# Kernel optimization log

Hardware: AMD Instinct MI355X
Metric: run time of the kernel (lower is better)

## Reference

```python
import jax, jax.numpy as jnp
import numpy as np

B, S, D, H = 4, 2048, 1024, 16
HD = D // H  # head_dim = 64


def setup_inputs() -> dict:
    key = jax.random.key(0)
    ks = jax.random.split(key, 5)
    scale = 0.02
    x = jax.random.normal(ks[0], (B, S, D), dtype=jnp.float32)
    W_qkv = jax.random.normal(ks[1], (D, 3 * D), dtype=jnp.float32) * scale
    b_qkv = jnp.zeros((3 * D,), dtype=jnp.float32)
    W_out = jax.random.normal(ks[2], (D, D), dtype=jnp.float32) * scale
    b_out = jnp.zeros((D,), dtype=jnp.float32)
    return {"x": x, "W_qkv": W_qkv, "b_qkv": b_qkv, "W_out": W_out, "b_out": b_out}


def reference(x, W_qkv, b_qkv, W_out, b_out):
    b, s, d = x.shape
    qkv = x @ W_qkv + b_qkv                      # [B,S,3D]
    q, k, v = jnp.split(qkv, 3, axis=-1)
    # [B,S,D] -> [B,H,S,hd]
    q = q.reshape(b, s, H, HD).transpose(0, 2, 1, 3)
    k = k.reshape(b, s, H, HD).transpose(0, 2, 1, 3)
    v = v.reshape(b, s, H, HD).transpose(0, 2, 1, 3)
    scores = jnp.einsum('bhqd,bhkd->bhqk', q, k) / jnp.sqrt(jnp.float32(HD))
    causal = jnp.tril(jnp.ones((s, s), dtype=bool))  # [S,S]
    scores = jnp.where(causal[None, None], scores, -jnp.inf)
    probs = jax.nn.softmax(scores, axis=-1)
    # dropout is identity in eval mode
    attn = jnp.einsum('bhqk,bhkd->bhqd', probs, v)  # [B,H,S,hd]
    attn = attn.transpose(0, 2, 1, 3).reshape(b, s, d)
    return attn @ W_out + b_out
```

## Files before the change

kernel.cpp:

```cpp
#include <hip/hip_runtime.h>


typedef short s16;
typedef __attribute__((ext_vector_type(4))) short s16x4;
typedef __attribute__((ext_vector_type(8))) short bf16x8;
typedef __attribute__((ext_vector_type(4))) float f32x4;

__device__ __forceinline__ s16 f2bf(float f) {
    union { float f; unsigned int i; } v;
    v.f = f;
    unsigned int r = v.i + 0x7fffu + ((v.i >> 16) & 1u);
    return (s16)(r >> 16);
}

__device__ __forceinline__ unsigned pack_bf16(float a, float b) {
    union { float f; unsigned u; } x, y;
    x.f = a; y.f = b;
    return __byte_perm(x.u + 0x8000u, y.u + 0x8000u, 0x7632);
}

__device__ __forceinline__ void load_lds16(const s16* g, s16* lds_base) {
    __builtin_amdgcn_global_load_lds(
        (const __attribute__((address_space(1))) void*)g,
        (__attribute__((address_space(3))) void*)lds_base, 16, 0, 0);
}

template <int N>
__device__ __forceinline__ void waitcnt_vm() {
    if constexpr (N == 0)      asm volatile("s_waitcnt vmcnt(0)" ::: "memory");
    else if constexpr (N == 3) asm volatile("s_waitcnt vmcnt(3)" ::: "memory");
    else if constexpr (N == 5) asm volatile("s_waitcnt vmcnt(5)" ::: "memory");
}

__global__ __launch_bounds__(256) void prep(
    const float* __restrict__ x,    s16* __restrict__ xo,
    const float* __restrict__ Wq,   s16* __restrict__ oq,
    const float* __restrict__ Wo,   s16* __restrict__ oo) {
    const int bid = blockIdx.x;
    const int tid = threadIdx.x;
    if (bid < 8192) {
        const int i = (bid * 256 + tid) * 4;
        const float4 f = *(const float4*)(x + i);
        s16x4 r = {f2bf(f.x), f2bf(f.y), f2bf(f.z), f2bf(f.w)};
        *(s16x4*)(xo + i) = r;
        return;
    }
    __shared__ float tile[32][33];
    const float* in;
    s16* out;
    int C, bx, by;
    if (bid < 11264) {
        const int b = bid - 8192;
        in = Wq; out = oq; C = 3072; bx = b % 96; by = b / 96;
    } else {
        const int b = bid - 11264;
        in = Wo; out = oo; C = 1024; bx = b & 31; by = b >> 5;
    }
    const int R = 1024;
    const int cb = bx * 32, rb = by * 32;
    const int tx = tid & 31, ty = tid >> 5;
#pragma unroll
    for (int i = 0; i < 32; i += 8)
        tile[ty + i][tx] = in[(size_t)(rb + ty + i) * C + cb + tx];
    __syncthreads();
#pragma unroll
    for (int i = 0; i < 32; i += 8)
        out[(size_t)(cb + ty + i) * R + rb + tx] = f2bf(tile[tx][ty + i]);
}

template <bool OUT_F32, int ACH, int BCH, int NWN_L2, int MF, int NF>
__global__ __launch_bounds__(512, 2) void gemm_tb(
    const s16* __restrict__ A,
    const s16* __restrict__ Bt,
    const float* __restrict__ bias,
    void* __restrict__ Cv,
    int M, int N, int K, int gx) {
    constexpr int NWN   = 1 << NWN_L2;
    constexpr int LOADS = ACH + BCH;
    constexpr int ABUF  = ACH * 4096;
    constexpr int BBUF  = BCH * 4096;
    constexpr int BM = ACH * 128, BN = BCH * 128;
    static_assert(MF * 16 * (8 / NWN) == BM, "M geometry");
    static_assert(NF * 16 * NWN == BN, "N geometry");
    __shared__ __attribute__((aligned(16))) s16 As[3 * ABUF];
    __shared__ __attribute__((aligned(16))) s16 Bs[3 * BBUF];

    const int tid  = threadIdx.x;
    const int lane = tid & 63;
    const int wave = tid >> 6;
    const int l15  = lane & 15;
    const int quad = lane >> 4;
    const int wr   = wave >> NWN_L2;
    const int wc   = wave & (NWN - 1);

    const int cpx = (int)gridDim.x >> 3;
    const int bid = (int)blockIdx.x;
    const int swz = (bid & 7) * cpx + (bid >> 3);
    const int m0 = (swz / gx) * BM;
    const int n0 = (swz % gx) * BN;

    const int sr  = tid >> 2;
    const int gl  = tid & 3;
    const int gsw = gl ^ ((sr >> 1) & 3);
    const s16* Ag = A  + (size_t)(m0 + sr) * K + gsw * 8;
    const s16* Bg = Bt + (size_t)(n0 + sr) * K + gsw * 8;

#define STG(bufi, kt) do {                                                          \
    _Pragma("unroll")                                                               \
    for (int c = 0; c < ACH; ++c)                                                   \
        load_lds16(Ag + (size_t)c * 128 * K + (size_t)(kt) * 32,                    \
                   &As[(bufi) * ABUF + c * 4096 + wave * 512]);                     \
    _Pragma("unroll")                                                               \
    for (int c = 0; c < BCH; ++c)                                                   \
        load_lds16(Bg + (size_t)c * 128 * K + (size_t)(kt) * 32,                    \
                   &Bs[(bufi) * BBUF + c * 4096 + wave * 512]); } while (0)

    f32x4 acc[MF][NF];
#pragma unroll
    for (int i = 0; i < MF; ++i)
#pragma unroll
        for (int j = 0; j < NF; ++j)
            acc[i][j] = (f32x4){0.f, 0.f, 0.f, 0.f};

    const int nk = K >> 5;

    STG(0, 0);
    STG(1, 1);
    waitcnt_vm<LOADS>();
    __builtin_amdgcn_s_barrier();

    for (int t = 0; t < nk; ++t) {
        const int cur = t % 3;
        if (t + 2 < nk) STG((t + 2) % 3, t + 2);

        const s16* Ab = As + cur * ABUF;
        const s16* Bb = Bs + cur * BBUF;
        bf16x8 bf[NF];
#pragma unroll
        for (int nf = 0; nf < NF; ++nf) {
            const int row = wc * (NF * 16) + nf * 16 + l15;
            bf[nf] = *(const bf16x8*)(Bb + row * 32 + ((quad ^ ((row >> 1) & 3)) << 3));
        }
        __builtin_amdgcn_s_setprio(1);
#pragma unroll
        for (int mf = 0; mf < MF; ++mf) {
            const int row = wr * (MF * 16) + mf * 16 + l15;
            const bf16x8 af = *(const bf16x8*)(Ab + row * 32 + ((quad ^ ((row >> 1) & 3)) << 3));
#pragma unroll
            for (int nf = 0; nf < NF; ++nf)
                acc[mf][nf] = __builtin_amdgcn_mfma_f32_16x16x32_bf16(af, bf[nf], acc[mf][nf], 0, 0, 0);
        }
        __builtin_amdgcn_s_setprio(0);

        if (t + 2 < nk)      waitcnt_vm<LOADS>();
        else if (t + 1 < nk) waitcnt_vm<0>();
        if (t + 1 < nk) __builtin_amdgcn_s_barrier();
    }
#undef STG

    float bv[NF];
#pragma unroll
    for (int nf = 0; nf < NF; ++nf)
        bv[nf] = bias[n0 + wc * (NF * 16) + nf * 16 + l15];
#pragma unroll
    for (int mf = 0; mf < MF; ++mf) {
#pragma unroll
        for (int r = 0; r < 4; ++r) {
            const int row = m0 + wr * (MF * 16) + mf * 16 + quad * 4 + r;
#pragma unroll
            for (int nf = 0; nf < NF; ++nf) {
                const int col = n0 + wc * (NF * 16) + nf * 16 + l15;
                const float v = acc[mf][nf][r] + bv[nf];
                if constexpr (OUT_F32)
                    ((float*)Cv)[(size_t)row * N + col] = v;
                else
                    ((s16*)Cv)[(size_t)row * N + col] = f2bf(v);
            }
        }
    }
}

__global__ __launch_bounds__(256) void attn_fwd(
    const s16* __restrict__ qkv,
    s16* __restrict__ attn) {
    __shared__ __attribute__((aligned(16))) s16 Ks[64 * 72];
    __shared__ __attribute__((aligned(16))) s16 Vt[64 * 72];
    __shared__ __attribute__((aligned(16))) s16 PT[4][32][88];

    const int tid  = threadIdx.x;
    const int lane = tid & 63;
    const int wave = tid >> 6;
    const int l15  = lane & 15;
    const int quad = lane >> 4;

    const int bid = blockIdx.x;
    const int hi  = bid >> 8;
    const int a   = bid & 3;
    const int bh  = (bid >> 2) & 63;
    const int qbase = a * 2 + (hi >> 1);
    const int qt  = (hi & 1) ? 15 - qbase : qbase;

    const size_t rowbase = (size_t)(bh >> 4) * 2048;
    const int hoff = (bh & 15) * 64;
    const int kp  = tid >> 3;
    const int p_s = tid & 7;
    const int kg  = kp >> 2;

    const float C2 = 0.18033688011112042f;
    const float M2 = 12.0f;

    const int wq = qt * 128 + wave * 32;

    bf16x8 qf[2][2];
#pragma unroll
    for (int qs = 0; qs < 2; ++qs)
#pragma unroll
        for (int ks = 0; ks < 2; ++ks)
            qf[qs][ks] = *(const bf16x8*)(qkv + (rowbase + wq + qs * 16 + l15) * 3072 + hoff + ks * 32 + quad * 8);

    float l_lane[2] = {0.f, 0.f};
    f32x4 o[2][4];
#pragma unroll
    for (int qs = 0; qs < 2; ++qs)
#pragma unroll
        for (int hs = 0; hs < 4; ++hs)
            o[qs][hs] = (f32x4){0.f, 0.f, 0.f, 0.f};

    const int nkt = qt * 2 + 2;
    bf16x8 kv[2], vv[2];
#pragma unroll
    for (int dk = 0; dk < 2; ++dk) {
        const s16* g = qkv + (rowbase + 2 * kp + dk) * 3072 + hoff + p_s * 8;
        kv[dk] = *(const bf16x8*)(g + 1024);
        vv[dk] = *(const bf16x8*)(g + 2048);
    }

    for (int kt = 0; kt < nkt; ++kt) {
        const int k0 = kt * 64;
        __syncthreads();
#pragma unroll
        for (int dk = 0; dk < 2; ++dk)
            *(bf16x8*)(Ks + (2 * kp + dk) * 72 + p_s * 8) = kv[dk];
#pragma unroll
        for (int j = 0; j < 8; ++j) {
            const unsigned dw = (unsigned)(unsigned short)vv[0][j] |
                                ((unsigned)(unsigned short)vv[1][j] << 16);
            *(unsigned*)(Vt + (p_s * 8 + j) * 72 + ((kg ^ p_s) << 3) + (2 * kp & 7)) = dw;
        }
        __syncthreads();

        if (kt + 1 < nkt) {
#pragma unroll
            for (int dk = 0; dk < 2; ++dk) {
                const s16* g = qkv + (rowbase + k0 + 64 + 2 * kp + dk) * 3072 + hoff + p_s * 8;
                kv[dk] = *(const bf16x8*)(g + 1024);
                vv[dk] = *(const bf16x8*)(g + 2048);
            }
        }

        if (k0 > wq + 31) continue;

        f32x4 st[2][4];
#pragma unroll
        for (int qs = 0; qs < 2; ++qs)
#pragma unroll
            for (int kb = 0; kb < 4; ++kb)
                st[qs][kb] = (f32x4){0.f, 0.f, 0.f, 0.f};
        __builtin_amdgcn_s_setprio(1);
#pragma unroll
        for (int kb = 0; kb < 4; ++kb)
#pragma unroll
            for (int ks = 0; ks < 2; ++ks) {
                const bf16x8 kf = *(const bf16x8*)(Ks + (kb * 16 + l15) * 72 + ks * 32 + quad * 8);
#pragma unroll
                for (int qs = 0; qs < 2; ++qs)
                    st[qs][kb] = __builtin_amdgcn_mfma_f32_16x16x32_bf16(kf, qf[qs][ks], st[qs][kb], 0, 0, 0);
            }
        __builtin_amdgcn_s_setprio(0);

        const bool edge = (k0 + 63 > wq);
#pragma unroll
        for (int qs = 0; qs < 2; ++qs) {
            const int q = wq + qs * 16 + l15;
#pragma unroll
            for (int kb = 0; kb < 4; ++kb) {
                float p4[4];
#pragma unroll
                for (int r = 0; r < 4; ++r) {
                    float t = fmaf(st[qs][kb][r], C2, -M2);
                    if (edge) {
                        const int key = k0 + kb * 16 + quad * 4 + r;
                        t = (key <= q) ? t : -150.f;
                    }
                    p4[r] = __builtin_amdgcn_exp2f(t);
                    l_lane[qs] += p4[r];
                }
                uint2 dd;
                dd.x = pack_bf16(p4[0], p4[1]);
                dd.y = pack_bf16(p4[2], p4[3]);
                *(uint2*)(&PT[wave][qs * 16 + l15][kb * 16 + quad * 4]) = dd;
            }
        }

        __builtin_amdgcn_s_setprio(1);
#pragma unroll
        for (int kk = 0; kk < 2; ++kk) {
            bf16x8 pf[2];
#pragma unroll
            for (int qs = 0; qs < 2; ++qs)
                pf[qs] = *(const bf16x8*)(&PT[wave][qs * 16 + l15][kk * 32 + quad * 8]);
#pragma unroll
            for (int hs = 0; hs < 4; ++hs) {
                const bf16x8 vf = *(const bf16x8*)(
                    Vt + (hs * 16 + l15) * 72 + (((kk * 4 + quad) ^ (2 * hs + (l15 >> 3))) << 3));
#pragma unroll
                for (int qs = 0; qs < 2; ++qs)
                    o[qs][hs] = __builtin_amdgcn_mfma_f32_16x16x32_bf16(vf, pf[qs], o[qs][hs], 0, 0, 0);
            }
        }
        __builtin_amdgcn_s_setprio(0);
    }

    float rl[2];
#pragma unroll
    for (int qs = 0; qs < 2; ++qs) {
        float l = l_lane[qs];
        l += __shfl_xor(l, 16);
        l += __shfl_xor(l, 32);
        rl[qs] = 1.f / l;
    }

#pragma unroll
    for (int qs = 0; qs < 2; ++qs) {
        const int q = wq + qs * 16 + l15;
#pragma unroll
        for (int hs = 0; hs < 4; ++hs) {
            uint2 dd;
            dd.x = pack_bf16(o[qs][hs][0] * rl[qs], o[qs][hs][1] * rl[qs]);
            dd.y = pack_bf16(o[qs][hs][2] * rl[qs], o[qs][hs][3] * rl[qs]);
            *(uint2*)(attn + (rowbase + q) * 1024 + hoff + hs * 16 + quad * 4) = dd;
        }
    }
}

extern "C" void kernel_launch(void* const* d_in, const int* in_sizes, int n_in,
                              void* d_out, int out_size, void* d_ws, size_t ws_size,
                              hipStream_t stream) {
    const float* x    = (const float*)d_in[0];
    const float* Wqkv = (const float*)d_in[1];
    const float* bqkv = (const float*)d_in[2];
    const float* Wout = (const float*)d_in[3];
    const float* bout = (const float*)d_in[4];
    float* out = (float*)d_out;

    s16* ws   = (s16*)d_ws;
    s16* qkv  = ws;
    s16* xba  = qkv + (size_t)8192 * 3072;
    s16* wtq  = xba + (size_t)8192 * 1024;
    s16* wto  = wtq + (size_t)3072 * 1024;

    prep<<<12288, 256, 0, stream>>>(x, xba, Wqkv, wtq, Wout, wto);
    gemm_tb<false, 2, 3, 2, 8, 6><<<256, 512, 0, stream>>>(
        xba, wtq, bqkv, qkv, 8192, 3072, 1024, 8);
    attn_fwd<<<1024, 256, 0, stream>>>(qkv, xba);
    gemm_tb<true, 2, 1, 1, 4, 4><<<256, 512, 0, stream>>>(
        xba, wto, bout, out, 8192, 1024, 1024, 8);
}
```

Baseline: 258.6 us.

## Replace GEMM with 4-slot ring-buffered, split-phase pipelined kernel

```diff
diff --git a/kernel.cpp b/kernel.cpp
--- a/kernel.cpp
+++ b/kernel.cpp
@@ -29,7 +29,7 @@
 __device__ __forceinline__ void waitcnt_vm() {
     if constexpr (N == 0)      asm volatile("s_waitcnt vmcnt(0)" ::: "memory");
     else if constexpr (N == 3) asm volatile("s_waitcnt vmcnt(3)" ::: "memory");
-    else if constexpr (N == 5) asm volatile("s_waitcnt vmcnt(5)" ::: "memory");
+    else if constexpr (N == 4) asm volatile("s_waitcnt vmcnt(4)" ::: "memory");
 }
 
 __global__ __launch_bounds__(256) void prep(
@@ -68,35 +68,33 @@
         out[(size_t)(cb + ty + i) * R + rb + tx] = f2bf(tile[tx][ty + i]);
 }
 
-template <bool OUT_F32, int ACH, int BCH, int NWN_L2, int MF, int NF>
-__global__ __launch_bounds__(512, 2) void gemm_tb(
+template <bool OUT_F32, int BCH>
+__global__ __launch_bounds__(512, 2) void gemm_ring(
     const s16* __restrict__ A,
     const s16* __restrict__ Bt,
     const float* __restrict__ bias,
     void* __restrict__ Cv,
     int M, int N, int K, int gx) {
-    constexpr int NWN   = 1 << NWN_L2;
-    constexpr int LOADS = ACH + BCH;
-    constexpr int ABUF  = ACH * 4096;
-    constexpr int BBUF  = BCH * 4096;
-    constexpr int BM = ACH * 128, BN = BCH * 128;
-    static_assert(MF * 16 * (8 / NWN) == BM, "M geometry");
-    static_assert(NF * 16 * NWN == BN, "N geometry");
-    __shared__ __attribute__((aligned(16))) s16 As[3 * ABUF];
-    __shared__ __attribute__((aligned(16))) s16 Bs[3 * BBUF];
+    constexpr int BN    = BCH * 128;
+    constexpr int NF    = BCH * 2;
+    constexpr int LPK   = 2 + BCH;
+    constexpr int ASLOT = 256 * 32;
+    constexpr int BSLOT = BN * 32;
+    __shared__ __attribute__((aligned(16))) s16 As[4 * ASLOT];
+    __shared__ __attribute__((aligned(16))) s16 Bs[4 * BSLOT];
 
     const int tid  = threadIdx.x;
     const int lane = tid & 63;
     const int wave = tid >> 6;
     const int l15  = lane & 15;
     const int quad = lane >> 4;
-    const int wr   = wave >> NWN_L2;
-    const int wc   = wave & (NWN - 1);
+    const int wr   = wave >> 2;
+    const int wc   = wave & 3;
 
     const int cpx = (int)gridDim.x >> 3;
     const int bid = (int)blockIdx.x;
     const int swz = (bid & 7) * cpx + (bid >> 3);
-    const int m0 = (swz / gx) * BM;
+    const int m0 = (swz / gx) * 256;
     const int n0 = (swz % gx) * BN;
 
     const int sr  = tid >> 2;
@@ -105,68 +103,87 @@
     const s16* Ag = A  + (size_t)(m0 + sr) * K + gsw * 8;
     const s16* Bg = Bt + (size_t)(n0 + sr) * K + gsw * 8;
 
-#define STG(bufi, kt) do {                                                          \
-    _Pragma("unroll")                                                               \
-    for (int c = 0; c < ACH; ++c)                                                   \
-        load_lds16(Ag + (size_t)c * 128 * K + (size_t)(kt) * 32,                    \
-                   &As[(bufi) * ABUF + c * 4096 + wave * 512]);                     \
-    _Pragma("unroll")                                                               \
-    for (int c = 0; c < BCH; ++c)                                                   \
-        load_lds16(Bg + (size_t)c * 128 * K + (size_t)(kt) * 32,                    \
-                   &Bs[(bufi) * BBUF + c * 4096 + wave * 512]); } while (0)
-
-    f32x4 acc[MF][NF];
-#pragma unroll
-    for (int i = 0; i < MF; ++i)
+    auto stgA = [&](int slot, int kt) {
+        load_lds16(Ag + (size_t)kt * 32,           &As[slot * ASLOT + wave * 512]);
+        load_lds16(Ag + (size_t)128 * K + kt * 32, &As[slot * ASLOT + 4096 + wave * 512]);
+    };
+    auto stgB = [&](int slot, int kt) {
+        load_lds16(Bg + (size_t)kt * 32, &Bs[slot * BSLOT + wave * 512]);
+        if constexpr (BCH == 2)
+            load_lds16(Bg + (size_t)128 * K + kt * 32, &Bs[slot * BSLOT + 4096 + wave * 512]);
+    };
+
+    f32x4 acc[8][NF];
+#pragma unroll
+    for (int i = 0; i < 8; ++i)
 #pragma unroll
         for (int j = 0; j < NF; ++j)
             acc[i][j] = (f32x4){0.f, 0.f, 0.f, 0.f};
 
     const int nk = K >> 5;
-
-    STG(0, 0);
-    STG(1, 1);
-    waitcnt_vm<LOADS>();
+    const int gr = ((quad ^ ((l15 >> 1) & 3)) << 3);
+
+    stgA(0, 0); stgB(0, 0);
+    stgA(1, 1); stgB(1, 1);
+    waitcnt_vm<LPK>();
     __builtin_amdgcn_s_barrier();
 
-    for (int t = 0; t < nk; ++t) {
-        const int cur = t % 3;
-        if (t + 2 < nk) STG((t + 2) % 3, t + 2);
-
-        const s16* Ab = As + cur * ABUF;
-        const s16* Bb = Bs + cur * BBUF;
-        bf16x8 bf[NF];
-#pragma unroll
-        for (int nf = 0; nf < NF; ++nf) {
-            const int row = wc * (NF * 16) + nf * 16 + l15;
-            bf[nf] = *(const bf16x8*)(Bb + row * 32 + ((quad ^ ((row >> 1) & 3)) << 3));
-        }
-        __builtin_amdgcn_s_setprio(1);
-#pragma unroll
-        for (int mf = 0; mf < MF; ++mf) {
-            const int row = wr * (MF * 16) + mf * 16 + l15;
-            const bf16x8 af = *(const bf16x8*)(Ab + row * 32 + ((quad ^ ((row >> 1) & 3)) << 3));
+    for (int tq = 0; tq < nk; tq += 4) {
+#pragma unroll
+        for (int u = 0; u < 4; ++u) {
+            const int t = tq + u;
+            const s16* Ab = As + u * ASLOT;
+            const s16* Bb = Bs + u * BSLOT;
+            const bool pre = (t + 2 < nk);
+            const int ns = (t + 2) & 3;
+
+            bf16x8 bf[NF], af[4];
 #pragma unroll
             for (int nf = 0; nf < NF; ++nf)
-                acc[mf][nf] = __builtin_amdgcn_mfma_f32_16x16x32_bf16(af, bf[nf], acc[mf][nf], 0, 0, 0);
-        }
-        __builtin_amdgcn_s_setprio(0);
-
-        if (t + 2 < nk)      waitcnt_vm<LOADS>();
-        else if (t + 1 < nk) waitcnt_vm<0>();
-        if (t + 1 < nk) __builtin_amdgcn_s_barrier();
-    }
-#undef STG
+                bf[nf] = *(const bf16x8*)(Bb + (wc * (NF * 16) + nf * 16 + l15) * 32 + gr);
+#pragma unroll
+            for (int mf = 0; mf < 4; ++mf)
+                af[mf] = *(const bf16x8*)(Ab + (wr * 128 + mf * 16 + l15) * 32 + gr);
+            if (pre) stgA(ns, t + 2);
+            __builtin_amdgcn_s_barrier();
+            __builtin_amdgcn_s_setprio(1);
+#pragma unroll
+            for (int mf = 0; mf < 4; ++mf)
+#pragma unroll
+                for (int nf = 0; nf < NF; ++nf)
+                    acc[mf][nf] = __builtin_amdgcn_mfma_f32_16x16x32_bf16(
+                        af[mf], bf[nf], acc[mf][nf], 0, 0, 0);
+            __builtin_amdgcn_s_setprio(0);
+            __builtin_amdgcn_s_barrier();
+
+#pragma unroll
+            for (int mf = 0; mf < 4; ++mf)
+                af[mf] = *(const bf16x8*)(Ab + (wr * 128 + (mf + 4) * 16 + l15) * 32 + gr);
+            if (pre) stgB(ns, t + 2);
+            __builtin_amdgcn_s_barrier();
+            __builtin_amdgcn_s_setprio(1);
+#pragma unroll
+            for (int mf = 0; mf < 4; ++mf)
+#pragma unroll
+                for (int nf = 0; nf < NF; ++nf)
+                    acc[mf + 4][nf] = __builtin_amdgcn_mfma_f32_16x16x32_bf16(
+                        af[mf], bf[nf], acc[mf + 4][nf], 0, 0, 0);
+            __builtin_amdgcn_s_setprio(0);
+            if (t < nk - 2)      waitcnt_vm<LPK>();
+            else if (t == nk - 2) waitcnt_vm<0>();
+            __builtin_amdgcn_s_barrier();
+        }
+    }
 
     float bv[NF];
 #pragma unroll
     for (int nf = 0; nf < NF; ++nf)
         bv[nf] = bias[n0 + wc * (NF * 16) + nf * 16 + l15];
 #pragma unroll
-    for (int mf = 0; mf < MF; ++mf) {
+    for (int mf = 0; mf < 8; ++mf) {
 #pragma unroll
         for (int r = 0; r < 4; ++r) {
-            const int row = m0 + wr * (MF * 16) + mf * 16 + quad * 4 + r;
+            const int row = m0 + wr * 128 + mf * 16 + quad * 4 + r;
 #pragma unroll
             for (int nf = 0; nf < NF; ++nf) {
                 const int col = n0 + wc * (NF * 16) + nf * 16 + l15;
@@ -360,9 +377,9 @@
     s16* wto  = wtq + (size_t)3072 * 1024;
 
     prep<<<12288, 256, 0, stream>>>(x, xba, Wqkv, wtq, Wout, wto);
-    gemm_tb<false, 2, 3, 2, 8, 6><<<256, 512, 0, stream>>>(
-        xba, wtq, bqkv, qkv, 8192, 3072, 1024, 8);
+    gemm_ring<false, 2><<<384, 512, 0, stream>>>(
+        xba, wtq, bqkv, qkv, 8192, 3072, 1024, 12);
     attn_fwd<<<1024, 256, 0, stream>>>(qkv, xba);
-    gemm_tb<true, 2, 1, 1, 4, 4><<<256, 512, 0, stream>>>(
+    gemm_ring<true, 1><<<256, 512, 0, stream>>>(
         xba, wto, bout, out, 8192, 1024, 1024, 8);
 }
```

After: 261.1 us. About the same (+1.0%).
